# Optimization experiments

Measured on AMD Instinct MI355X. Metric: run time of the kernel, lower is better.

Reference implementation:

```python
import jax, jax.numpy as jnp
import numpy as np

N = 262144
D = 128
E = 524288
N_PHYS = 5
EPS_SL = 1e-8
EPS_LN = 1e-5


def _signed_log(x):
    return jnp.sign(x) * jnp.log(jnp.abs(x) + EPS_SL)


def setup_inputs() -> dict:
    key = jax.random.key(0)
    ks = jax.random.split(key, 12)
    h = jax.random.normal(ks[0], (N, D), dtype=jnp.float32)
    c1 = jax.random.normal(ks[1], (N,), dtype=jnp.float32)
    c2 = jax.random.normal(ks[2], (N,), dtype=jnp.float32)
    c3 = jax.random.normal(ks[3], (N,), dtype=jnp.float32)
    c4 = jax.random.normal(ks[4], (N,), dtype=jnp.float32)
    q_new = jax.random.normal(ks[5], (N,), dtype=jnp.float32)
    src = jax.random.randint(ks[6], (E,), 0, N, dtype=jnp.int64)
    dst = jax.random.randint(ks[7], (E,), 0, N, dtype=jnp.int64)
    d_in = 2 * D + N_PHYS
    W1 = jax.random.normal(ks[8], (d_in, D), dtype=jnp.float32) / np.sqrt(d_in)
    b1 = jnp.zeros((D,), dtype=jnp.float32)
    W2 = jax.random.normal(ks[9], (D, D), dtype=jnp.float32) / np.sqrt(D)
    b2 = jnp.zeros((D,), dtype=jnp.float32)
    gamma = jnp.ones((D,), dtype=jnp.float32)
    beta = jnp.zeros((D,), dtype=jnp.float32)
    return {"h": h, "c1_next_upstream": c1, "c2_prev_upstream": c2,
            "c3_self": c3, "c4_lateral": c4, "q_new": q_new,
            "src": src, "dst": dst,
            "W1": W1, "b1": b1, "W2": W2, "b2": b2,
            "gamma": gamma, "beta": beta}


def reference(h, c1_next_upstream, c2_prev_upstream, c3_self, c4_lateral,
              q_new, src, dst, W1, b1, W2, b2, gamma, beta):
    # sparse adjacency matmul: upstream_h[i] = sum_{j: j->i} h[j]
    upstream_h = jax.ops.segment_sum(h[src], dst, num_segments=h.shape[0])
    phys = jnp.stack([_signed_log(c1_next_upstream),
                      _signed_log(c2_prev_upstream),
                      _signed_log(c3_self),
                      _signed_log(c4_lateral),
                      _signed_log(q_new)], axis=-1)  # (N, 5)
    node_input = jnp.concatenate([h, upstream_h, phys], axis=-1)  # (N, 2D+5)
    hid = jax.nn.silu(node_input @ W1 + b1)
    mlp_out = hid @ W2 + b2
    z = h + mlp_out
    mean = jnp.mean(z, axis=-1, keepdims=True)
    var = jnp.var(z, axis=-1, keepdims=True)
    return (z - mean) * jax.lax.rsqrt(var + EPS_LN) * gamma + beta
```

## Files before the change

kernel.cpp:

```cpp
#include <hip/hip_runtime.h>
#include <math.h>

#define NN 262144
#define DD 128
#define EPS_SL 1e-8f
#define EPS_LN 1e-5f
#define THREADS 512
#define TILE_M 64
#define NBLOCKS 256
#define NTILES (NN / TILE_M)
#define TPB (NTILES / NBLOCKS)

typedef __attribute__((ext_vector_type(8))) short bf16x8;
typedef __attribute__((ext_vector_type(4))) float f32x4;

#define OFF_W1 0
#define OFF_W2 73728
#define OFF_X  106496
#define OFF_H  143360
#define OFF_RED 159744
#define SMEM_TOT 161792

#define WS_OFFS   0
#define WS_CURSOR 1048832
#define WS_BSUM   2097408
#define WS_ESRC   2101504
#define WS_NEEDED (2101504 + 524288 * 4)

__device__ inline unsigned short f2bf(float f) {
    union { float f; unsigned int i; } v; v.f = f;
    unsigned int r = v.i + 0x7fffu + ((v.i >> 16) & 1u);
    return (unsigned short)(r >> 16);
}
__device__ inline unsigned int pack2(float a, float b) {
    return (unsigned int)f2bf(a) | ((unsigned int)f2bf(b) << 16);
}
__device__ inline uint4 pack8(float4 a, float4 b) {
    return make_uint4(pack2(a.x, a.y), pack2(a.z, a.w),
                      pack2(b.x, b.y), pack2(b.z, b.w));
}
__device__ inline float signed_log(float x) {
    float l = __logf(fabsf(x) + EPS_SL);
    return (x > 0.f) ? l : ((x < 0.f) ? -l : 0.f);
}
__device__ inline void stx(unsigned short* sX, int kb, int row, uint4 v) {
    *(uint4*)(sX + (((kb * 64 + row) ^ (kb & 7)) * 8)) = v;
}
__device__ inline bf16x8 ldx(const unsigned short* sX, int kb, int row) {
    return *(const bf16x8*)(sX + (((kb * 64 + row) ^ (kb & 7)) * 8));
}

__global__ void hist_kernel(const int* __restrict__ dst, int* counts, int E) {
    int e = blockIdx.x * blockDim.x + threadIdx.x;
    if (e < E) atomicAdd(&counts[dst[e]], 1);
}

__global__ void scan_local(int* offs, int* bsum) {
    __shared__ int tmp[256];
    int t = threadIdx.x, i = blockIdx.x * 256 + t;
    int own = offs[i];
    tmp[t] = own;
    __syncthreads();
    for (int off = 1; off < 256; off <<= 1) {
        int v = (t >= off) ? tmp[t - off] : 0;
        __syncthreads();
        tmp[t] += v;
        __syncthreads();
    }
    offs[i] = tmp[t] - own;
    if (t == 255) bsum[blockIdx.x] = tmp[255];
}

__global__ void scan_bsum(int* bsum) {
    __shared__ int tmp[1024];
    int t = threadIdx.x;
    int own = bsum[t];
    tmp[t] = own;
    __syncthreads();
    for (int off = 1; off < 1024; off <<= 1) {
        int v = (t >= off) ? tmp[t - off] : 0;
        __syncthreads();
        tmp[t] += v;
        __syncthreads();
    }
    bsum[t] = tmp[t] - own;
}

__global__ void scan_fixup(int* offs, const int* __restrict__ bsum, int* cursor, int E) {
    int i = blockIdx.x * 256 + threadIdx.x;
    int v = offs[i] + bsum[i >> 8];
    offs[i] = v;
    cursor[i] = v;
    if (i == 0) offs[NN] = E;
}

__global__ void fill_kernel(const int* __restrict__ src, const int* __restrict__ dst,
                            int* cursor, int* esrc, int E) {
    int e = blockIdx.x * blockDim.x + threadIdx.x;
    if (e < E) {
        int p = atomicAdd(&cursor[dst[e]], 1);
        esrc[p] = src[e];
    }
}

__global__ __launch_bounds__(256) void gather_kernel(
    const float4* __restrict__ h4, const int* __restrict__ offs,
    const int* __restrict__ esrc, char* outb)
{
    int stride = gridDim.x * 256;
    for (int idx = blockIdx.x * 256 + threadIdx.x; idx < NN * 16; idx += stride) {
        int n = idx >> 4, c = idx & 15;
        int o0 = offs[n], o1 = offs[n + 1];
        float4 a = make_float4(0.f, 0.f, 0.f, 0.f);
        float4 b = make_float4(0.f, 0.f, 0.f, 0.f);
        for (int e = o0; e < o1; ++e) {
            const float4* hr = h4 + (size_t)esrc[e] * 32 + c * 2;
            float4 p0 = hr[0], p1 = hr[1];
            a.x += p0.x; a.y += p0.y; a.z += p0.z; a.w += p0.w;
            b.x += p1.x; b.y += p1.y; b.z += p1.z; b.w += p1.w;
        }
        *(uint4*)(outb + (size_t)n * 512 + c * 16) = pack8(a, b);
    }
}

__global__ void scatter_kernel(const float4* __restrict__ h4,
                               const int* __restrict__ src,
                               const int* __restrict__ dst,
                               float* up, int E) {
    int tid = blockIdx.x * blockDim.x + threadIdx.x;
    int e = tid >> 5;
    if (e >= E) return;
    int c = tid & 31;
    float4 v = h4[(size_t)src[e] * 32 + c];
    float* o = up + (size_t)dst[e] * DD + c * 4;
    atomicAdd(o + 0, v.x);
    atomicAdd(o + 1, v.y);
    atomicAdd(o + 2, v.z);
    atomicAdd(o + 3, v.w);
}

template <int GATHER>
__global__ __launch_bounds__(THREADS) void node_kernel(
    const float* __restrict__ h, const void* up,
    const float* __restrict__ c1, const float* __restrict__ c2,
    const float* __restrict__ c3, const float* __restrict__ c4,
    const float* __restrict__ qn,
    const float* __restrict__ W1, const float* __restrict__ b1,
    const float* __restrict__ W2, const float* __restrict__ b2,
    const float* __restrict__ gamma, const float* __restrict__ beta,
    float* out)
{
    extern __shared__ char smem[];
    unsigned short* sW1 = (unsigned short*)(smem + OFF_W1);
    unsigned short* sW2 = (unsigned short*)(smem + OFF_W2);
    unsigned short* sX  = (unsigned short*)(smem + OFF_X);
    unsigned short* sH  = (unsigned short*)(smem + OFF_H);
    float2* red = (float2*)(smem + OFF_RED);

    const int tid = threadIdx.x;

    for (int c = tid; c < 36 * 128; c += THREADS) {
        int kb = c >> 7, n = c & 127;
        unsigned short tmp[8] __attribute__((aligned(16)));
        #pragma unroll
        for (int j = 0; j < 8; ++j) {
            int k = kb * 8 + j;
            tmp[j] = (k < 261) ? f2bf(W1[k * DD + n]) : (unsigned short)0;
        }
        *(uint4*)(sW1 + c * 8) = *(const uint4*)tmp;
    }
    for (int c = tid; c < 16 * 128; c += THREADS) {
        int kb = c >> 7, n = c & 127;
        unsigned short tmp[8] __attribute__((aligned(16)));
        #pragma unroll
        for (int j = 0; j < 8; ++j) tmp[j] = f2bf(W2[(kb * 8 + j) * DD + n]);
        *(uint4*)(sW2 + c * 8) = *(const uint4*)tmp;
    }
    if (tid < 192) {
        int kb = 33 + (tid >> 6), row = tid & 63;
        stx(sX, kb, row, make_uint4(0u, 0u, 0u, 0u));
    }

    const int lane = tid & 63;
    const int w    = tid >> 6;
    const int wm   = w >> 2;
    const int wn   = w & 3;
    const int l15  = lane & 15;
    const int lk   = lane >> 4;
    const int col0 = wn * 32 + l15;
    const int col1 = col0 + 16;

    const float b1v[2] = {b1[col0], b1[col1]};
    const float b2v[2] = {b2[col0], b2[col1]};
    const float gv[2]  = {gamma[col0], gamma[col1]};
    const float bv[2]  = {beta[col0], beta[col1]};

    const bf16x8* W1f = (const bf16x8*)sW1;
    const bf16x8* Hf  = (const bf16x8*)sH;
    const bf16x8* W2f = (const bf16x8*)sW2;

    const int k0 = tid & 15;
    const int r0 = tid >> 4;

    float4 h0a, h0b, h1a, h1b;
    uint4  u0, u1;
    float4 v0a, v0b, v1a, v1b;
    float pc1 = 0.f, pc2 = 0.f, pc3 = 0.f, pc4 = 0.f, pc5 = 0.f;

    {
        int base = blockIdx.x * TPB * TILE_M;
        const float* hp = h + (size_t)(base + r0) * DD + k0 * 8;
        h0a = *(const float4*)hp;       h0b = *(const float4*)(hp + 4);
        h1a = *(const float4*)(hp + 32 * DD); h1b = *(const float4*)(hp + 32 * DD + 4);
        if (GATHER) {
            const char* ub = (const char*)up;
            u0 = *(const uint4*)(ub + (size_t)(base + r0) * 512 + k0 * 16);
            u1 = *(const uint4*)(ub + (size_t)(base + r0 + 32) * 512 + k0 * 16);
        } else {
            const float* uf = (const float*)up + (size_t)(base + r0) * DD + k0 * 8;
            v0a = *(const float4*)uf;       v0b = *(const float4*)(uf + 4);
            v1a = *(const float4*)(uf + 32 * DD); v1b = *(const float4*)(uf + 32 * DD + 4);
        }
        if (tid < 64) {
            int n0 = base + tid;
            pc1 = c1[n0]; pc2 = c2[n0]; pc3 = c3[n0]; pc4 = c4[n0]; pc5 = qn[n0];
        }
    }
    __syncthreads();

    for (int tt = 0; tt < TPB; ++tt) {
        const int base = (blockIdx.x * TPB + tt) * TILE_M;

        stx(sX, k0, r0,      pack8(h0a, h0b));
        stx(sX, k0, r0 + 32, pack8(h1a, h1b));
        if (GATHER) {
            stx(sX, 16 + k0, r0,      u0);
            stx(sX, 16 + k0, r0 + 32, u1);
        } else {
            stx(sX, 16 + k0, r0,      pack8(v0a, v0b));
            stx(sX, 16 + k0, r0 + 32, pack8(v1a, v1b));
        }
        if (tid < 64) {
            uint4 pv = make_uint4(pack2(signed_log(pc1), signed_log(pc2)),
                                  pack2(signed_log(pc3), signed_log(pc4)),
                                  pack2(signed_log(pc5), 0.f), 0u);
            stx(sX, 32, tid, pv);
        }

        if (tt + 1 < TPB) {
            int bn = base + TILE_M;
            const float* hp = h + (size_t)(bn + r0) * DD + k0 * 8;
            h0a = *(const float4*)hp;       h0b = *(const float4*)(hp + 4);
            h1a = *(const float4*)(hp + 32 * DD); h1b = *(const float4*)(hp + 32 * DD + 4);
            if (GATHER) {
                const char* ub = (const char*)up;
                u0 = *(const uint4*)(ub + (size_t)(bn + r0) * 512 + k0 * 16);
                u1 = *(const uint4*)(ub + (size_t)(bn + r0 + 32) * 512 + k0 * 16);
            } else {
                const float* uf = (const float*)up + (size_t)(bn + r0) * DD + k0 * 8;
                v0a = *(const float4*)uf;       v0b = *(const float4*)(uf + 4);
                v1a = *(const float4*)(uf + 32 * DD); v1b = *(const float4*)(uf + 32 * DD + 4);
            }
            if (tid < 64) {
                int n0 = bn + tid;
                pc1 = c1[n0]; pc2 = c2[n0]; pc3 = c3[n0]; pc4 = c4[n0]; pc5 = qn[n0];
            }
        }
        __syncthreads();

        f32x4 acc[2][2] = {};
        #pragma unroll
        for (int ks = 0; ks < 9; ++ks) {
            int kb = ks * 4 + lk;
            bf16x8 a0  = ldx(sX, kb, wm * 32 + l15);
            bf16x8 a1  = ldx(sX, kb, wm * 32 + 16 + l15);
            bf16x8 bb0 = W1f[kb * 128 + col0];
            bf16x8 bb1 = W1f[kb * 128 + col1];
            acc[0][0] = __builtin_amdgcn_mfma_f32_16x16x32_bf16(a0, bb0, acc[0][0], 0, 0, 0);
            acc[0][1] = __builtin_amdgcn_mfma_f32_16x16x32_bf16(a0, bb1, acc[0][1], 0, 0, 0);
            acc[1][0] = __builtin_amdgcn_mfma_f32_16x16x32_bf16(a1, bb0, acc[1][0], 0, 0, 0);
            acc[1][1] = __builtin_amdgcn_mfma_f32_16x16x32_bf16(a1, bb1, acc[1][1], 0, 0, 0);
        }
        #pragma unroll
        for (int fm = 0; fm < 2; ++fm) {
            int row = wm * 32 + fm * 16 + lk * 4;
            #pragma unroll
            for (int fn = 0; fn < 2; ++fn) {
                int col = wn * 32 + fn * 16 + l15;
                int kbh = col >> 3, ko = col & 7;
                #pragma unroll
                for (int r = 0; r < 4; ++r) {
                    float v = acc[fm][fn][r] + b1v[fn];
                    float sg = 1.f / (1.f + __expf(-v));
                    sH[(kbh * 64 + row + r) * 8 + ko] = f2bf(v * sg);
                }
            }
        }
        __syncthreads();

        f32x4 acc2[2][2] = {};
        #pragma unroll
        for (int ks = 0; ks < 4; ++ks) {
            int kb = ks * 4 + lk;
            bf16x8 a0  = Hf[kb * 64 + wm * 32 + l15];
            bf16x8 a1  = Hf[kb * 64 + wm * 32 + 16 + l15];
            bf16x8 bb0 = W2f[kb * 128 + col0];
            bf16x8 bb1 = W2f[kb * 128 + col1];
            acc2[0][0] = __builtin_amdgcn_mfma_f32_16x16x32_bf16(a0, bb0, acc2[0][0], 0, 0, 0);
            acc2[0][1] = __builtin_amdgcn_mfma_f32_16x16x32_bf16(a0, bb1, acc2[0][1], 0, 0, 0);
            acc2[1][0] = __builtin_amdgcn_mfma_f32_16x16x32_bf16(a1, bb0, acc2[1][0], 0, 0, 0);
            acc2[1][1] = __builtin_amdgcn_mfma_f32_16x16x32_bf16(a1, bb1, acc2[1][1], 0, 0, 0);
        }

        float rs1[2][4], rs2[2][4];
        #pragma unroll
        for (int fm = 0; fm < 2; ++fm) {
            #pragma unroll
            for (int r = 0; r < 4; ++r) {
                size_t rowg = (size_t)(base + wm * 32 + fm * 16 + lk * 4 + r) * DD;
                float z0 = acc2[fm][0][r] + b2v[0] + h[rowg + col0];
                float z1 = acc2[fm][1][r] + b2v[1] + h[rowg + col1];
                acc2[fm][0][r] = z0; acc2[fm][1][r] = z1;
                float s = z0 + z1, q = z0 * z0 + z1 * z1;
                #pragma unroll
                for (int off = 1; off < 16; off <<= 1) {
                    s += __shfl_xor(s, off);
                    q += __shfl_xor(q, off);
                }
                rs1[fm][r] = s; rs2[fm][r] = q;
            }
        }
        if (l15 == 0) {
            #pragma unroll
            for (int fm = 0; fm < 2; ++fm)
                #pragma unroll
                for (int r = 0; r < 4; ++r)
                    red[wn * 64 + wm * 32 + fm * 16 + lk * 4 + r] =
                        make_float2(rs1[fm][r], rs2[fm][r]);
        }
        __syncthreads();

        #pragma unroll
        for (int fm = 0; fm < 2; ++fm) {
            #pragma unroll
            for (int r = 0; r < 4; ++r) {
                int rloc = wm * 32 + fm * 16 + lk * 4 + r;
                float2 t0 = red[rloc], t1 = red[64 + rloc],
                       t2 = red[128 + rloc], t3 = red[192 + rloc];
                float S = t0.x + t1.x + t2.x + t3.x;
                float Q = t0.y + t1.y + t2.y + t3.y;
                float mean = S * (1.f / 128.f);
                float var  = Q * (1.f / 128.f) - mean * mean;
                float rstd = rsqrtf(var + EPS_LN);
                size_t rowg = (size_t)(base + rloc) * DD;
                out[rowg + col0] = (acc2[fm][0][r] - mean) * rstd * gv[0] + bv[0];
                out[rowg + col1] = (acc2[fm][1][r] - mean) * rstd * gv[1] + bv[1];
            }
        }
    }
}

extern "C" void kernel_launch(void* const* d_in, const int* in_sizes, int n_in,
                              void* d_out, int out_size, void* d_ws, size_t ws_size,
                              hipStream_t stream) {
    const float* h     = (const float*)d_in[0];
    const float* c1    = (const float*)d_in[1];
    const float* c2    = (const float*)d_in[2];
    const float* c3    = (const float*)d_in[3];
    const float* c4    = (const float*)d_in[4];
    const float* qn    = (const float*)d_in[5];
    const int*   src   = (const int*)d_in[6];
    const int*   dst   = (const int*)d_in[7];
    const float* W1    = (const float*)d_in[8];
    const float* b1    = (const float*)d_in[9];
    const float* W2    = (const float*)d_in[10];
    const float* b2    = (const float*)d_in[11];
    const float* gamma = (const float*)d_in[12];
    const float* beta  = (const float*)d_in[13];
    float* out = (float*)d_out;
    int E = in_sizes[6];

    if (ws_size >= (size_t)WS_NEEDED) {
        char* ws = (char*)d_ws;
        int* offs   = (int*)(ws + WS_OFFS);
        int* cursor = (int*)(ws + WS_CURSOR);
        int* bsum   = (int*)(ws + WS_BSUM);
        int* esrc   = (int*)(ws + WS_ESRC);

        hipMemsetAsync(offs, 0, (size_t)NN * sizeof(int), stream);
        int eb = (E + 255) / 256;
        hist_kernel<<<eb, 256, 0, stream>>>(dst, offs, E);
        scan_local<<<NN / 256, 256, 0, stream>>>(offs, bsum);
        scan_bsum<<<1, 1024, 0, stream>>>(bsum);
        scan_fixup<<<NN / 256, 256, 0, stream>>>(offs, bsum, cursor, E);
        fill_kernel<<<eb, 256, 0, stream>>>(src, dst, cursor, esrc, E);

        gather_kernel<<<2048, 256, 0, stream>>>((const float4*)h, offs, esrc, (char*)d_out);

        hipFuncSetAttribute(reinterpret_cast<const void*>(&node_kernel<1>),
                            hipFuncAttributeMaxDynamicSharedMemorySize, SMEM_TOT);
        node_kernel<1><<<NBLOCKS, THREADS, SMEM_TOT, stream>>>(
            h, d_out, c1, c2, c3, c4, qn,
            W1, b1, W2, b2, gamma, beta, out);
    } else {
        hipMemsetAsync(d_out, 0, (size_t)NN * DD * sizeof(float), stream);
        int sthreads = E * 32;
        int sblocks = (sthreads + 255) / 256;
        scatter_kernel<<<sblocks, 256, 0, stream>>>((const float4*)h, src, dst, out, E);
        hipFuncSetAttribute(reinterpret_cast<const void*>(&node_kernel<0>),
                            hipFuncAttributeMaxDynamicSharedMemorySize, SMEM_TOT);
        node_kernel<0><<<NBLOCKS, THREADS, SMEM_TOT, stream>>>(
            h, d_out, c1, c2, c3, c4, qn,
            W1, b1, W2, b2, gamma, beta, out);
    }
}
```

Measured before the change: 232.6 us.

## Fuse CSR gather into node kernel and read pre-packed weights from global

Moves the per-node neighbour gather into the node kernel, so each block first sums its 512 nodes' neighbour rows into the bf16 staging area of the output buffer and then runs the MLP on them, removing a separate kernel launch. A new prep kernel converts W1/W2 to bf16 MFMA fragments once in workspace, and the MLP reads them from global/L2 instead of each block rebuilding them in LDS. LDS use drops from about 158KB to 54KB, allowing several blocks per CU (launch bounds 4) and 512 blocks. The cost is that weight fragments are now fetched from cache on every tile, and the gather phase no longer overlaps with the matmul within a block.

Measured after the change: 363.6 us. 1.56x slower.

```diff
diff --git a/kernel.cpp b/kernel.cpp
--- a/kernel.cpp
+++ b/kernel.cpp
@@ -7,25 +7,31 @@
 #define EPS_LN 1e-5f
 #define THREADS 512
 #define TILE_M 64
-#define NBLOCKS 256
-#define NTILES (NN / TILE_M)
-#define TPB (NTILES / NBLOCKS)
+#define NBLOCKS 512
+#define TPB 8
+#define NPB (TPB * TILE_M)
 
 typedef __attribute__((ext_vector_type(8))) short bf16x8;
 typedef __attribute__((ext_vector_type(4))) float f32x4;
 
-#define OFF_W1 0
-#define OFF_W2 73728
-#define OFF_X  106496
-#define OFF_H  143360
-#define OFF_RED 159744
-#define SMEM_TOT 161792
+#define OFF_X   0
+#define OFF_H   36864
+#define OFF_RED 53248
+#define SMEM_TOT 55296
+
+#define FB_OFF_W1 0
+#define FB_OFF_W2 73728
+#define FB_OFF_X  106496
+#define FB_OFF_H  143360
+#define FB_OFF_RED 159744
+#define FB_SMEM_TOT 161792
 
 #define WS_OFFS   0
 #define WS_CURSOR 1048832
 #define WS_BSUM   2097408
 #define WS_ESRC   2101504
-#define WS_NEEDED (2101504 + 524288 * 4)
+#define WS_WFRAG  4198656
+#define WS_NEEDED (4198656 + 106496)
 
 __device__ inline unsigned short f2bf(float f) {
     union { float f; unsigned int i; } v; v.f = f;
@@ -103,24 +109,24 @@
     }
 }
 
-__global__ __launch_bounds__(256) void gather_kernel(
-    const float4* __restrict__ h4, const int* __restrict__ offs,
-    const int* __restrict__ esrc, char* outb)
-{
-    int stride = gridDim.x * 256;
-    for (int idx = blockIdx.x * 256 + threadIdx.x; idx < NN * 16; idx += stride) {
-        int n = idx >> 4, c = idx & 15;
-        int o0 = offs[n], o1 = offs[n + 1];
-        float4 a = make_float4(0.f, 0.f, 0.f, 0.f);
-        float4 b = make_float4(0.f, 0.f, 0.f, 0.f);
-        for (int e = o0; e < o1; ++e) {
-            const float4* hr = h4 + (size_t)esrc[e] * 32 + c * 2;
-            float4 p0 = hr[0], p1 = hr[1];
-            a.x += p0.x; a.y += p0.y; a.z += p0.z; a.w += p0.w;
-            b.x += p1.x; b.y += p1.y; b.z += p1.z; b.w += p1.w;
-        }
-        *(uint4*)(outb + (size_t)n * 512 + c * 16) = pack8(a, b);
-    }
+__global__ void prep_weights(const float* __restrict__ W1, const float* __restrict__ W2,
+                             uint4* wfrag) {
+    int t = blockIdx.x * blockDim.x + threadIdx.x;
+    if (t >= 52 * 128) return;
+    int kb = t >> 7, n = t & 127;
+    unsigned short tmp[8] __attribute__((aligned(16)));
+    if (kb < 36) {
+        #pragma unroll
+        for (int j = 0; j < 8; ++j) {
+            int k = kb * 8 + j;
+            tmp[j] = (k < 261) ? f2bf(W1[k * DD + n]) : (unsigned short)0;
+        }
+    } else {
+        int kb2 = kb - 36;
+        #pragma unroll
+        for (int j = 0; j < 8; ++j) tmp[j] = f2bf(W2[(kb2 * 8 + j) * DD + n]);
+    }
+    wfrag[t] = *(const uint4*)tmp;
 }
 
 __global__ void scatter_kernel(const float4* __restrict__ h4,
@@ -139,9 +145,210 @@
     atomicAdd(o + 3, v.w);
 }
 
-template <int GATHER>
-__global__ __launch_bounds__(THREADS) void node_kernel(
-    const float* __restrict__ h, const void* up,
+__global__ __launch_bounds__(THREADS, 4) void node_kernel(
+    const float* __restrict__ h,
+    const int* __restrict__ offs, const int* __restrict__ esrc,
+    const uint4* __restrict__ wfrag,
+    const float* __restrict__ c1, const float* __restrict__ c2,
+    const float* __restrict__ c3, const float* __restrict__ c4,
+    const float* __restrict__ qn,
+    const float* __restrict__ b1, const float* __restrict__ b2,
+    const float* __restrict__ gamma, const float* __restrict__ beta,
+    float* out)
+{
+    extern __shared__ char smem[];
+    unsigned short* sX = (unsigned short*)(smem + OFF_X);
+    unsigned short* sH = (unsigned short*)(smem + OFF_H);
+    float2* red = (float2*)(smem + OFF_RED);
+
+    const int tid = threadIdx.x;
+    const int nbase = blockIdx.x * NPB;
+
+    if (tid < 192) stx(sX, 33 + (tid >> 6), tid & 63, make_uint4(0u, 0u, 0u, 0u));
+
+    {
+        char* outb = (char*)out;
+        for (int it = 0; it < NPB * 16 / THREADS; ++it) {
+            int idx = it * THREADS + tid;
+            int nl = idx >> 4, c = idx & 15;
+            int n = nbase + nl;
+            int o0 = offs[n], o1 = offs[n + 1];
+            float4 a = make_float4(0.f, 0.f, 0.f, 0.f);
+            float4 b = make_float4(0.f, 0.f, 0.f, 0.f);
+            for (int e = o0; e < o1; ++e) {
+                const float4* hr = (const float4*)h + (size_t)esrc[e] * 32 + c * 2;
+                float4 p0 = hr[0], p1 = hr[1];
+                a.x += p0.x; a.y += p0.y; a.z += p0.z; a.w += p0.w;
+                b.x += p1.x; b.y += p1.y; b.z += p1.z; b.w += p1.w;
+            }
+            *(uint4*)(outb + (size_t)n * 512 + c * 16) = pack8(a, b);
+        }
+    }
+    __syncthreads();
+
+    const int lane = tid & 63;
+    const int w    = tid >> 6;
+    const int wm   = w >> 2;
+    const int wn   = w & 3;
+    const int l15  = lane & 15;
+    const int lk   = lane >> 4;
+    const int col0 = wn * 32 + l15;
+    const int col1 = col0 + 16;
+
+    const float b1v[2] = {b1[col0], b1[col1]};
+    const float b2v[2] = {b2[col0], b2[col1]};
+    const float gv[2]  = {gamma[col0], gamma[col1]};
+    const float bv[2]  = {beta[col0], beta[col1]};
+
+    const int k0 = tid & 15;
+    const int r0 = tid >> 4;
+
+    float4 h0a, h0b, h1a, h1b;
+    uint4  u0, u1;
+    float pc1 = 0.f, pc2 = 0.f, pc3 = 0.f, pc4 = 0.f, pc5 = 0.f;
+
+    {
+        int base = nbase;
+        const float* hp = h + (size_t)(base + r0) * DD + k0 * 8;
+        h0a = *(const float4*)hp;             h0b = *(const float4*)(hp + 4);
+        h1a = *(const float4*)(hp + 32 * DD); h1b = *(const float4*)(hp + 32 * DD + 4);
+        const char* ub = (const char*)out;
+        u0 = *(const uint4*)(ub + (size_t)(base + r0) * 512 + k0 * 16);
+        u1 = *(const uint4*)(ub + (size_t)(base + r0 + 32) * 512 + k0 * 16);
+        if (tid < 64) {
+            int n0 = base + tid;
+            pc1 = c1[n0]; pc2 = c2[n0]; pc3 = c3[n0]; pc4 = c4[n0]; pc5 = qn[n0];
+        }
+    }
+
+    for (int tt = 0; tt < TPB; ++tt) {
+        const int base = nbase + tt * TILE_M;
+
+        stx(sX, k0, r0,      pack8(h0a, h0b));
+        stx(sX, k0, r0 + 32, pack8(h1a, h1b));
+        stx(sX, 16 + k0, r0,      u0);
+        stx(sX, 16 + k0, r0 + 32, u1);
+        if (tid < 64) {
+            uint4 pv = make_uint4(pack2(signed_log(pc1), signed_log(pc2)),
+                                  pack2(signed_log(pc3), signed_log(pc4)),
+                                  pack2(signed_log(pc5), 0.f), 0u);
+            stx(sX, 32, tid, pv);
+        }
+
+        if (tt + 1 < TPB) {
+            int bn = base + TILE_M;
+            const float* hp = h + (size_t)(bn + r0) * DD + k0 * 8;
+            h0a = *(const float4*)hp;             h0b = *(const float4*)(hp + 4);
+            h1a = *(const float4*)(hp + 32 * DD); h1b = *(const float4*)(hp + 32 * DD + 4);
+            const char* ub = (const char*)out;
+            u0 = *(const uint4*)(ub + (size_t)(bn + r0) * 512 + k0 * 16);
+            u1 = *(const uint4*)(ub + (size_t)(bn + r0 + 32) * 512 + k0 * 16);
+            if (tid < 64) {
+                int n0 = bn + tid;
+                pc1 = c1[n0]; pc2 = c2[n0]; pc3 = c3[n0]; pc4 = c4[n0]; pc5 = qn[n0];
+            }
+        }
+        __syncthreads();
+
+        int zoff = 0;
+        asm volatile("" : "+v"(zoff));
+        const uint4* wf1 = wfrag + zoff;
+        const uint4* wf2 = wfrag + 36 * 128 + zoff;
+
+        f32x4 acc[2][2] = {};
+        #pragma unroll
+        for (int ks = 0; ks < 9; ++ks) {
+            int kb = ks * 4 + lk;
+            bf16x8 a0  = ldx(sX, kb, wm * 32 + l15);
+            bf16x8 a1  = ldx(sX, kb, wm * 32 + 16 + l15);
+            bf16x8 bb0 = *(const bf16x8*)(wf1 + kb * 128 + col0);
+            bf16x8 bb1 = *(const bf16x8*)(wf1 + kb * 128 + col1);
+            acc[0][0] = __builtin_amdgcn_mfma_f32_16x16x32_bf16(a0, bb0, acc[0][0], 0, 0, 0);
+            acc[0][1] = __builtin_amdgcn_mfma_f32_16x16x32_bf16(a0, bb1, acc[0][1], 0, 0, 0);
+            acc[1][0] = __builtin_amdgcn_mfma_f32_16x16x32_bf16(a1, bb0, acc[1][0], 0, 0, 0);
+            acc[1][1] = __builtin_amdgcn_mfma_f32_16x16x32_bf16(a1, bb1, acc[1][1], 0, 0, 0);
+        }
+        #pragma unroll
+        for (int fm = 0; fm < 2; ++fm) {
+            int row = wm * 32 + fm * 16 + lk * 4;
+            #pragma unroll
+            for (int fn = 0; fn < 2; ++fn) {
+                int col = wn * 32 + fn * 16 + l15;
+                int kbh = col >> 3, ko = col & 7;
+                #pragma unroll
+                for (int r = 0; r < 4; ++r) {
+                    float v = acc[fm][fn][r] + b1v[fn];
+                    float sg = 1.f / (1.f + __expf(-v));
+                    sH[(kbh * 64 + row + r) * 8 + ko] = f2bf(v * sg);
+                }
+            }
+        }
+        __syncthreads();
+
+        f32x4 acc2[2][2] = {};
+        #pragma unroll
+        for (int ks = 0; ks < 4; ++ks) {
+            int kb = ks * 4 + lk;
+            bf16x8 a0  = *(const bf16x8*)(sH + (kb * 64 + wm * 32 + l15) * 8);
+            bf16x8 a1  = *(const bf16x8*)(sH + (kb * 64 + wm * 32 + 16 + l15) * 8);
+            bf16x8 bb0 = *(const bf16x8*)(wf2 + kb * 128 + col0);
+            bf16x8 bb1 = *(const bf16x8*)(wf2 + kb * 128 + col1);
+            acc2[0][0] = __builtin_amdgcn_mfma_f32_16x16x32_bf16(a0, bb0, acc2[0][0], 0, 0, 0);
+            acc2[0][1] = __builtin_amdgcn_mfma_f32_16x16x32_bf16(a0, bb1, acc2[0][1], 0, 0, 0);
+            acc2[1][0] = __builtin_amdgcn_mfma_f32_16x16x32_bf16(a1, bb0, acc2[1][0], 0, 0, 0);
+            acc2[1][1] = __builtin_amdgcn_mfma_f32_16x16x32_bf16(a1, bb1, acc2[1][1], 0, 0, 0);
+        }
+
+        float rs1[2][4], rs2[2][4];
+        #pragma unroll
+        for (int fm = 0; fm < 2; ++fm) {
+            #pragma unroll
+            for (int r = 0; r < 4; ++r) {
+                size_t rowg = (size_t)(base + wm * 32 + fm * 16 + lk * 4 + r) * DD;
+                float z0 = acc2[fm][0][r] + b2v[0] + h[rowg + col0];
+                float z1 = acc2[fm][1][r] + b2v[1] + h[rowg + col1];
+                acc2[fm][0][r] = z0; acc2[fm][1][r] = z1;
+                float s = z0 + z1, q = z0 * z0 + z1 * z1;
+                #pragma unroll
+                for (int off = 1; off < 16; off <<= 1) {
+                    s += __shfl_xor(s, off);
+                    q += __shfl_xor(q, off);
+                }
+                rs1[fm][r] = s; rs2[fm][r] = q;
+            }
+        }
+        if (l15 == 0) {
+            #pragma unroll
+            for (int fm = 0; fm < 2; ++fm)
+                #pragma unroll
+                for (int r = 0; r < 4; ++r)
+                    red[wn * 64 + wm * 32 + fm * 16 + lk * 4 + r] =
+                        make_float2(rs1[fm][r], rs2[fm][r]);
+        }
+        __syncthreads();
+
+        #pragma unroll
+        for (int fm = 0; fm < 2; ++fm) {
+            #pragma unroll
+            for (int r = 0; r < 4; ++r) {
+                int rloc = wm * 32 + fm * 16 + lk * 4 + r;
+                float2 t0 = red[rloc], t1 = red[64 + rloc],
+                       t2 = red[128 + rloc], t3 = red[192 + rloc];
+                float S = t0.x + t1.x + t2.x + t3.x;
+                float Q = t0.y + t1.y + t2.y + t3.y;
+                float mean = S * (1.f / 128.f);
+                float var  = Q * (1.f / 128.f) - mean * mean;
+                float rstd = rsqrtf(var + EPS_LN);
+                size_t rowg = (size_t)(base + rloc) * DD;
+                out[rowg + col0] = (acc2[fm][0][r] - mean) * rstd * gv[0] + bv[0];
+                out[rowg + col1] = (acc2[fm][1][r] - mean) * rstd * gv[1] + bv[1];
+            }
+        }
+    }
+}
+
+__global__ __launch_bounds__(THREADS) void node_kernel_fb(
+    const float* __restrict__ h, const float* up,
     const float* __restrict__ c1, const float* __restrict__ c2,
     const float* __restrict__ c3, const float* __restrict__ c4,
     const float* __restrict__ qn,
@@ -151,11 +358,11 @@
     float* out)
 {
     extern __shared__ char smem[];
-    unsigned short* sW1 = (unsigned short*)(smem + OFF_W1);
-    unsigned short* sW2 = (unsigned short*)(smem + OFF_W2);
-    unsigned short* sX  = (unsigned short*)(smem + OFF_X);
-    unsigned short* sH  = (unsigned short*)(smem + OFF_H);
-    float2* red = (float2*)(smem + OFF_RED);
+    unsigned short* sW1 = (unsigned short*)(smem + FB_OFF_W1);
+    unsigned short* sW2 = (unsigned short*)(smem + FB_OFF_W2);
+    unsigned short* sX  = (unsigned short*)(smem + FB_OFF_X);
+    unsigned short* sH  = (unsigned short*)(smem + FB_OFF_H);
+    float2* red = (float2*)(smem + FB_OFF_RED);
 
     const int tid = threadIdx.x;
 
@@ -201,26 +408,20 @@
 
     const int k0 = tid & 15;
     const int r0 = tid >> 4;
+    const int FB_TPB = NN / TILE_M / NBLOCKS;
 
     float4 h0a, h0b, h1a, h1b;
-    uint4  u0, u1;
     float4 v0a, v0b, v1a, v1b;
     float pc1 = 0.f, pc2 = 0.f, pc3 = 0.f, pc4 = 0.f, pc5 = 0.f;
 
     {
-        int base = blockIdx.x * TPB * TILE_M;
+        int base = blockIdx.x * FB_TPB * TILE_M;
         const float* hp = h + (size_t)(base + r0) * DD + k0 * 8;
-        h0a = *(const float4*)hp;       h0b = *(const float4*)(hp + 4);
+        h0a = *(const float4*)hp;             h0b = *(const float4*)(hp + 4);
         h1a = *(const float4*)(hp + 32 * DD); h1b = *(const float4*)(hp + 32 * DD + 4);
-        if (GATHER) {
-            const char* ub = (const char*)up;
-            u0 = *(const uint4*)(ub + (size_t)(base + r0) * 512 + k0 * 16);
-            u1 = *(const uint4*)(ub + (size_t)(base + r0 + 32) * 512 + k0 * 16);
-        } else {
-            const float* uf = (const float*)up + (size_t)(base + r0) * DD + k0 * 8;
-            v0a = *(const float4*)uf;       v0b = *(const float4*)(uf + 4);
-            v1a = *(const float4*)(uf + 32 * DD); v1b = *(const float4*)(uf + 32 * DD + 4);
-        }
+        const float* uf = up + (size_t)(base + r0) * DD + k0 * 8;
+        v0a = *(const float4*)uf;             v0b = *(const float4*)(uf + 4);
+        v1a = *(const float4*)(uf + 32 * DD); v1b = *(const float4*)(uf + 32 * DD + 4);
         if (tid < 64) {
             int n0 = base + tid;
             pc1 = c1[n0]; pc2 = c2[n0]; pc3 = c3[n0]; pc4 = c4[n0]; pc5 = qn[n0];
@@ -228,39 +429,27 @@
     }
     __syncthreads();
 
-    for (int tt = 0; tt < TPB; ++tt) {
-        const int base = (blockIdx.x * TPB + tt) * TILE_M;
+    for (int tt = 0; tt < FB_TPB; ++tt) {
+        const int base = (blockIdx.x * FB_TPB + tt) * TILE_M;
 
         stx(sX, k0, r0,      pack8(h0a, h0b));
         stx(sX, k0, r0 + 32, pack8(h1a, h1b));
-        if (GATHER) {
-            stx(sX, 16 + k0, r0,      u0);
-            stx(sX, 16 + k0, r0 + 32, u1);
-        } else {
-            stx(sX, 16 + k0, r0,      pack8(v0a, v0b));
-            stx(sX, 16 + k0, r0 + 32, pack8(v1a, v1b));
-        }
+        stx(sX, 16 + k0, r0,      pack8(v0a, v0b));
+        stx(sX, 16 + k0, r0 + 32, pack8(v1a, v1b));
         if (tid < 64) {
             uint4 pv = make_uint4(pack2(signed_log(pc1), signed_log(pc2)),
                                   pack2(signed_log(pc3), signed_log(pc4)),
                                   pack2(signed_log(pc5), 0.f), 0u);
             stx(sX, 32, tid, pv);
         }
-
-        if (tt + 1 < TPB) {
+        if (tt + 1 < FB_TPB) {
             int bn = base + TILE_M;
             const float* hp = h + (size_t)(bn + r0) * DD + k0 * 8;
-            h0a = *(const float4*)hp;       h0b = *(const float4*)(hp + 4);
+            h0a = *(const float4*)hp;             h0b = *(const float4*)(hp + 4);
             h1a = *(const float4*)(hp + 32 * DD); h1b = *(const float4*)(hp + 32 * DD + 4);
-            if (GATHER) {
-                const char* ub = (const char*)up;
-                u0 = *(const uint4*)(ub + (size_t)(bn + r0) * 512 + k0 * 16);
-                u1 = *(const uint4*)(ub + (size_t)(bn + r0 + 32) * 512 + k0 * 16);
-            } else {
-                const float* uf = (const float*)up + (size_t)(bn + r0) * DD + k0 * 8;
-                v0a = *(const float4*)uf;       v0b = *(const float4*)(uf + 4);
-                v1a = *(const float4*)(uf + 32 * DD); v1b = *(const float4*)(uf + 32 * DD + 4);
-            }
+            const float* uf = up + (size_t)(bn + r0) * DD + k0 * 8;
+            v0a = *(const float4*)uf;             v0b = *(const float4*)(uf + 4);
+            v1a = *(const float4*)(uf + 32 * DD); v1b = *(const float4*)(uf + 32 * DD + 4);
             if (tid < 64) {
                 int n0 = bn + tid;
                 pc1 = c1[n0]; pc2 = c2[n0]; pc3 = c3[n0]; pc4 = c4[n0]; pc5 = qn[n0];
@@ -386,6 +575,7 @@
         int* cursor = (int*)(ws + WS_CURSOR);
         int* bsum   = (int*)(ws + WS_BSUM);
         int* esrc   = (int*)(ws + WS_ESRC);
+        uint4* wfrag = (uint4*)(ws + WS_WFRAG);
 
         hipMemsetAsync(offs, 0, (size_t)NN * sizeof(int), stream);
         int eb = (E + 255) / 256;
@@ -394,23 +584,20 @@
         scan_bsum<<<1, 1024, 0, stream>>>(bsum);
         scan_fixup<<<NN / 256, 256, 0, stream>>>(offs, bsum, cursor, E);
         fill_kernel<<<eb, 256, 0, stream>>>(src, dst, cursor, esrc, E);
-
-        gather_kernel<<<2048, 256, 0, stream>>>((const float4*)h, offs, esrc, (char*)d_out);
-
-        hipFuncSetAttribute(reinterpret_cast<const void*>(&node_kernel<1>),
-                            hipFuncAttributeMaxDynamicSharedMemorySize, SMEM_TOT);
-        node_kernel<1><<<NBLOCKS, THREADS, SMEM_TOT, stream>>>(
-            h, d_out, c1, c2, c3, c4, qn,
-            W1, b1, W2, b2, gamma, beta, out);
+        prep_weights<<<26, 256, 0, stream>>>(W1, W2, wfrag);
+
+        node_kernel<<<NBLOCKS, THREADS, SMEM_TOT, stream>>>(
+            h, offs, esrc, wfrag, c1, c2, c3, c4, qn,
+            b1, b2, gamma, beta, out);
     } else {
         hipMemsetAsync(d_out, 0, (size_t)NN * DD * sizeof(float), stream);
         int sthreads = E * 32;
         int sblocks = (sthreads + 255) / 256;
         scatter_kernel<<<sblocks, 256, 0, stream>>>((const float4*)h, src, dst, out, E);
-        hipFuncSetAttribute(reinterpret_cast<const void*>(&node_kernel<0>),
-                            hipFuncAttributeMaxDynamicSharedMemorySize, SMEM_TOT);
-        node_kernel<0><<<NBLOCKS, THREADS, SMEM_TOT, stream>>>(
-            h, d_out, c1, c2, c3, c4, qn,
+        hipFuncSetAttribute(reinterpret_cast<const void*>(&node_kernel_fb),
+                            hipFuncAttributeMaxDynamicSharedMemorySize, FB_SMEM_TOT);
+        node_kernel_fb<<<NBLOCKS, THREADS, FB_SMEM_TOT, stream>>>(
+            h, out, c1, c2, c3, c4, qn,
             W1, b1, W2, b2, gamma, beta, out);
     }
 }
```

## Double node kernel threads to 1024 with one 16-row MFMA strip per wave

Applied to the files above, without the earlier changes.

Raises the node kernel block size from 512 to 1024 threads so each of the 16 waves handles a 16-row by 32-column fragment instead of 32 rows. Each thread now loads one row-chunk of h and upstream rather than two. The work per wave is halved to expose more parallelism and latency hiding within the block. In exchange there is less B-operand reuse per wave, the W1/W2 fragments are re-read from LDS by more waves, and there are more waves per barrier. Two further edits are not about speed: the workspace size check now derives from E, and launch bounds gain a minimum-blocks hint.

Result: slower. 241.9 us (+4.0%).

```diff
diff --git a/kernel.cpp b/kernel.cpp
--- a/kernel.cpp
+++ b/kernel.cpp
@@ -5,7 +5,7 @@
 #define DD 128
 #define EPS_SL 1e-8f
 #define EPS_LN 1e-5f
-#define THREADS 512
+#define THREADS 1024
 #define TILE_M 64
 #define NBLOCKS 256
 #define NTILES (NN / TILE_M)
@@ -25,7 +25,6 @@
 #define WS_CURSOR 1048832
 #define WS_BSUM   2097408
 #define WS_ESRC   2101504
-#define WS_NEEDED (2101504 + 524288 * 4)
 
 __device__ inline unsigned short f2bf(float f) {
     union { float f; unsigned int i; } v; v.f = f;
@@ -140,7 +139,7 @@
 }
 
 template <int GATHER>
-__global__ __launch_bounds__(THREADS) void node_kernel(
+__global__ __launch_bounds__(THREADS, 4) void node_kernel(
     const float* __restrict__ h, const void* up,
     const float* __restrict__ c1, const float* __restrict__ c2,
     const float* __restrict__ c3, const float* __restrict__ c4,
@@ -202,24 +201,21 @@
     const int k0 = tid & 15;
     const int r0 = tid >> 4;
 
-    float4 h0a, h0b, h1a, h1b;
-    uint4  u0, u1;
-    float4 v0a, v0b, v1a, v1b;
+    float4 h0a, h0b;
+    uint4  u0;
+    float4 v0a, v0b;
     float pc1 = 0.f, pc2 = 0.f, pc3 = 0.f, pc4 = 0.f, pc5 = 0.f;
 
     {
         int base = blockIdx.x * TPB * TILE_M;
         const float* hp = h + (size_t)(base + r0) * DD + k0 * 8;
-        h0a = *(const float4*)hp;       h0b = *(const float4*)(hp + 4);
-        h1a = *(const float4*)(hp + 32 * DD); h1b = *(const float4*)(hp + 32 * DD + 4);
+        h0a = *(const float4*)hp; h0b = *(const float4*)(hp + 4);
         if (GATHER) {
             const char* ub = (const char*)up;
             u0 = *(const uint4*)(ub + (size_t)(base + r0) * 512 + k0 * 16);
-            u1 = *(const uint4*)(ub + (size_t)(base + r0 + 32) * 512 + k0 * 16);
         } else {
             const float* uf = (const float*)up + (size_t)(base + r0) * DD + k0 * 8;
-            v0a = *(const float4*)uf;       v0b = *(const float4*)(uf + 4);
-            v1a = *(const float4*)(uf + 32 * DD); v1b = *(const float4*)(uf + 32 * DD + 4);
+            v0a = *(const float4*)uf; v0b = *(const float4*)(uf + 4);
         }
         if (tid < 64) {
             int n0 = base + tid;
@@ -231,15 +227,9 @@
     for (int tt = 0; tt < TPB; ++tt) {
         const int base = (blockIdx.x * TPB + tt) * TILE_M;
 
-        stx(sX, k0, r0,      pack8(h0a, h0b));
-        stx(sX, k0, r0 + 32, pack8(h1a, h1b));
-        if (GATHER) {
-            stx(sX, 16 + k0, r0,      u0);
-            stx(sX, 16 + k0, r0 + 32, u1);
-        } else {
-            stx(sX, 16 + k0, r0,      pack8(v0a, v0b));
-            stx(sX, 16 + k0, r0 + 32, pack8(v1a, v1b));
-        }
+        stx(sX, k0, r0, pack8(h0a, h0b));
+        if (GATHER) stx(sX, 16 + k0, r0, u0);
+        else        stx(sX, 16 + k0, r0, pack8(v0a, v0b));
         if (tid < 64) {
             uint4 pv = make_uint4(pack2(signed_log(pc1), signed_log(pc2)),
                                   pack2(signed_log(pc3), signed_log(pc4)),
@@ -250,16 +240,13 @@
         if (tt + 1 < TPB) {
             int bn = base + TILE_M;
             const float* hp = h + (size_t)(bn + r0) * DD + k0 * 8;
-            h0a = *(const float4*)hp;       h0b = *(const float4*)(hp + 4);
-            h1a = *(const float4*)(hp + 32 * DD); h1b = *(const float4*)(hp + 32 * DD + 4);
+            h0a = *(const float4*)hp; h0b = *(const float4*)(hp + 4);
             if (GATHER) {
                 const char* ub = (const char*)up;
                 u0 = *(const uint4*)(ub + (size_t)(bn + r0) * 512 + k0 * 16);
-                u1 = *(const uint4*)(ub + (size_t)(bn + r0 + 32) * 512 + k0 * 16);
             } else {
                 const float* uf = (const float*)up + (size_t)(bn + r0) * DD + k0 * 8;
-                v0a = *(const float4*)uf;       v0b = *(const float4*)(uf + 4);
-                v1a = *(const float4*)(uf + 32 * DD); v1b = *(const float4*)(uf + 32 * DD + 4);
+                v0a = *(const float4*)uf; v0b = *(const float4*)(uf + 4);
             }
             if (tid < 64) {
                 int n0 = bn + tid;
@@ -268,29 +255,25 @@
         }
         __syncthreads();
 
-        f32x4 acc[2][2] = {};
+        f32x4 acc[2] = {};
         #pragma unroll
         for (int ks = 0; ks < 9; ++ks) {
             int kb = ks * 4 + lk;
-            bf16x8 a0  = ldx(sX, kb, wm * 32 + l15);
-            bf16x8 a1  = ldx(sX, kb, wm * 32 + 16 + l15);
+            bf16x8 a   = ldx(sX, kb, wm * 16 + l15);
             bf16x8 bb0 = W1f[kb * 128 + col0];
             bf16x8 bb1 = W1f[kb * 128 + col1];
-            acc[0][0] = __builtin_amdgcn_mfma_f32_16x16x32_bf16(a0, bb0, acc[0][0], 0, 0, 0);
-            acc[0][1] = __builtin_amdgcn_mfma_f32_16x16x32_bf16(a0, bb1, acc[0][1], 0, 0, 0);
-            acc[1][0] = __builtin_amdgcn_mfma_f32_16x16x32_bf16(a1, bb0, acc[1][0], 0, 0, 0);
-            acc[1][1] = __builtin_amdgcn_mfma_f32_16x16x32_bf16(a1, bb1, acc[1][1], 0, 0, 0);
-        }
-        #pragma unroll
-        for (int fm = 0; fm < 2; ++fm) {
-            int row = wm * 32 + fm * 16 + lk * 4;
+            acc[0] = __builtin_amdgcn_mfma_f32_16x16x32_bf16(a, bb0, acc[0], 0, 0, 0);
+            acc[1] = __builtin_amdgcn_mfma_f32_16x16x32_bf16(a, bb1, acc[1], 0, 0, 0);
+        }
+        {
+            int row = wm * 16 + lk * 4;
             #pragma unroll
             for (int fn = 0; fn < 2; ++fn) {
                 int col = wn * 32 + fn * 16 + l15;
                 int kbh = col >> 3, ko = col & 7;
                 #pragma unroll
                 for (int r = 0; r < 4; ++r) {
-                    float v = acc[fm][fn][r] + b1v[fn];
+                    float v = acc[fn][r] + b1v[fn];
                     float sg = 1.f / (1.f + __expf(-v));
                     sH[(kbh * 64 + row + r) * 8 + ko] = f2bf(v * sg);
                 }
@@ -298,64 +281,52 @@
         }
         __syncthreads();
 
-        f32x4 acc2[2][2] = {};
+        f32x4 acc2[2] = {};
         #pragma unroll
         for (int ks = 0; ks < 4; ++ks) {
             int kb = ks * 4 + lk;
-            bf16x8 a0  = Hf[kb * 64 + wm * 32 + l15];
-            bf16x8 a1  = Hf[kb * 64 + wm * 32 + 16 + l15];
+            bf16x8 a   = Hf[kb * 64 + wm * 16 + l15];
             bf16x8 bb0 = W2f[kb * 128 + col0];
             bf16x8 bb1 = W2f[kb * 128 + col1];
-            acc2[0][0] = __builtin_amdgcn_mfma_f32_16x16x32_bf16(a0, bb0, acc2[0][0], 0, 0, 0);
-            acc2[0][1] = __builtin_amdgcn_mfma_f32_16x16x32_bf16(a0, bb1, acc2[0][1], 0, 0, 0);
-            acc2[1][0] = __builtin_amdgcn_mfma_f32_16x16x32_bf16(a1, bb0, acc2[1][0], 0, 0, 0);
-            acc2[1][1] = __builtin_amdgcn_mfma_f32_16x16x32_bf16(a1, bb1, acc2[1][1], 0, 0, 0);
-        }
-
-        float rs1[2][4], rs2[2][4];
-        #pragma unroll
-        for (int fm = 0; fm < 2; ++fm) {
+            acc2[0] = __builtin_amdgcn_mfma_f32_16x16x32_bf16(a, bb0, acc2[0], 0, 0, 0);
+            acc2[1] = __builtin_amdgcn_mfma_f32_16x16x32_bf16(a, bb1, acc2[1], 0, 0, 0);
+        }
+
+        float rs1[4], rs2[4];
+        #pragma unroll
+        for (int r = 0; r < 4; ++r) {
+            size_t rowg = (size_t)(base + wm * 16 + lk * 4 + r) * DD;
+            float z0 = acc2[0][r] + b2v[0] + h[rowg + col0];
+            float z1 = acc2[1][r] + b2v[1] + h[rowg + col1];
+            acc2[0][r] = z0; acc2[1][r] = z1;
+            float s = z0 + z1, q = z0 * z0 + z1 * z1;
             #pragma unroll
-            for (int r = 0; r < 4; ++r) {
-                size_t rowg = (size_t)(base + wm * 32 + fm * 16 + lk * 4 + r) * DD;
-                float z0 = acc2[fm][0][r] + b2v[0] + h[rowg + col0];
-                float z1 = acc2[fm][1][r] + b2v[1] + h[rowg + col1];
-                acc2[fm][0][r] = z0; acc2[fm][1][r] = z1;
-                float s = z0 + z1, q = z0 * z0 + z1 * z1;
-                #pragma unroll
-                for (int off = 1; off < 16; off <<= 1) {
-                    s += __shfl_xor(s, off);
-                    q += __shfl_xor(q, off);
-                }
-                rs1[fm][r] = s; rs2[fm][r] = q;
+            for (int off = 1; off < 16; off <<= 1) {
+                s += __shfl_xor(s, off);
+                q += __shfl_xor(q, off);
             }
+            rs1[r] = s; rs2[r] = q;
         }
         if (l15 == 0) {
             #pragma unroll
-            for (int fm = 0; fm < 2; ++fm)
-                #pragma unroll
-                for (int r = 0; r < 4; ++r)
-                    red[wn * 64 + wm * 32 + fm * 16 + lk * 4 + r] =
-                        make_float2(rs1[fm][r], rs2[fm][r]);
-        }
-        __syncthreads();
-
-        #pragma unroll
-        for (int fm = 0; fm < 2; ++fm) {
-            #pragma unroll
-            for (int r = 0; r < 4; ++r) {
-                int rloc = wm * 32 + fm * 16 + lk * 4 + r;
-                float2 t0 = red[rloc], t1 = red[64 + rloc],
-                       t2 = red[128 + rloc], t3 = red[192 + rloc];
-                float S = t0.x + t1.x + t2.x + t3.x;
-                float Q = t0.y + t1.y + t2.y + t3.y;
-                float mean = S * (1.f / 128.f);
-                float var  = Q * (1.f / 128.f) - mean * mean;
-                float rstd = rsqrtf(var + EPS_LN);
-                size_t rowg = (size_t)(base + rloc) * DD;
-                out[rowg + col0] = (acc2[fm][0][r] - mean) * rstd * gv[0] + bv[0];
-                out[rowg + col1] = (acc2[fm][1][r] - mean) * rstd * gv[1] + bv[1];
-            }
+            for (int r = 0; r < 4; ++r)
+                red[wn * 64 + wm * 16 + lk * 4 + r] = make_float2(rs1[r], rs2[r]);
+        }
+        __syncthreads();
+
+        #pragma unroll
+        for (int r = 0; r < 4; ++r) {
+            int rloc = wm * 16 + lk * 4 + r;
+            float2 t0 = red[rloc], t1 = red[64 + rloc],
+                   t2 = red[128 + rloc], t3 = red[192 + rloc];
+            float S = t0.x + t1.x + t2.x + t3.x;
+            float Q = t0.y + t1.y + t2.y + t3.y;
+            float mean = S * (1.f / 128.f);
+            float var  = Q * (1.f / 128.f) - mean * mean;
+            float rstd = rsqrtf(var + EPS_LN);
+            size_t rowg = (size_t)(base + rloc) * DD;
+            out[rowg + col0] = (acc2[0][r] - mean) * rstd * gv[0] + bv[0];
+            out[rowg + col1] = (acc2[1][r] - mean) * rstd * gv[1] + bv[1];
         }
     }
 }
@@ -379,8 +350,9 @@
     const float* beta  = (const float*)d_in[13];
     float* out = (float*)d_out;
     int E = in_sizes[6];
-
-    if (ws_size >= (size_t)WS_NEEDED) {
+    size_t ws_needed = (size_t)WS_ESRC + (size_t)E * 4;
+
+    if (ws_size >= ws_needed) {
         char* ws = (char*)d_ws;
         int* offs   = (int*)(ws + WS_OFFS);
         int* cursor = (int*)(ws + WS_CURSOR);
```

## Pack bf16 h alongside gathered sums; read residual from shared memory

Applied to the files above, without the earlier changes.

The gather kernel now also writes a bf16 copy of each node's own h row into the second half of its 512-byte output slot, which previously went unused. The node kernel then loads both halves from that staging buffer instead of reading fp32 h twice (once for the MLP input, once for the residual). The residual is now read back from the bf16 tile in shared memory. This cuts global reads in the node kernel at the cost of extra h reads and writes in the gather pass, and the residual loses precision by using bf16 instead of fp32 h.

Result: slower. 261.4 us (+12.4%).

```diff
diff --git a/kernel.cpp b/kernel.cpp
--- a/kernel.cpp
+++ b/kernel.cpp
@@ -25,13 +25,15 @@
 #define WS_CURSOR 1048832
 #define WS_BSUM   2097408
 #define WS_ESRC   2101504
-#define WS_NEEDED (2101504 + 524288 * 4)
 
 __device__ inline unsigned short f2bf(float f) {
     union { float f; unsigned int i; } v; v.f = f;
     unsigned int r = v.i + 0x7fffu + ((v.i >> 16) & 1u);
     return (unsigned short)(r >> 16);
 }
+__device__ inline float bf2f(unsigned short u) {
+    union { float f; unsigned int i; } v; v.i = ((unsigned int)u) << 16; return v.f;
+}
 __device__ inline unsigned int pack2(float a, float b) {
     return (unsigned int)f2bf(a) | ((unsigned int)f2bf(b) << 16);
 }
@@ -48,6 +50,9 @@
 }
 __device__ inline bf16x8 ldx(const unsigned short* sX, int kb, int row) {
     return *(const bf16x8*)(sX + (((kb * 64 + row) ^ (kb & 7)) * 8));
+}
+__device__ inline float ldx_elem(const unsigned short* sX, int kb, int row, int e) {
+    return bf2f(sX[(((kb * 64 + row) ^ (kb & 7)) * 8) + e]);
 }
 
 __global__ void hist_kernel(const int* __restrict__ dst, int* counts, int E) {
@@ -119,7 +124,11 @@
             a.x += p0.x; a.y += p0.y; a.z += p0.z; a.w += p0.w;
             b.x += p1.x; b.y += p1.y; b.z += p1.z; b.w += p1.w;
         }
-        *(uint4*)(outb + (size_t)n * 512 + c * 16) = pack8(a, b);
+        const float4* hn = h4 + (size_t)n * 32 + c * 2;
+        float4 q0 = hn[0], q1 = hn[1];
+        char* slot = outb + (size_t)n * 512;
+        *(uint4*)(slot + c * 16)       = pack8(a, b);
+        *(uint4*)(slot + 256 + c * 16) = pack8(q0, q1);
     }
 }
 
@@ -202,23 +211,25 @@
     const int k0 = tid & 15;
     const int r0 = tid >> 4;
 
+    uint4 hu0, hu1, uu0, uu1;
     float4 h0a, h0b, h1a, h1b;
-    uint4  u0, u1;
     float4 v0a, v0b, v1a, v1b;
     float pc1 = 0.f, pc2 = 0.f, pc3 = 0.f, pc4 = 0.f, pc5 = 0.f;
 
     {
         int base = blockIdx.x * TPB * TILE_M;
-        const float* hp = h + (size_t)(base + r0) * DD + k0 * 8;
-        h0a = *(const float4*)hp;       h0b = *(const float4*)(hp + 4);
-        h1a = *(const float4*)(hp + 32 * DD); h1b = *(const float4*)(hp + 32 * DD + 4);
         if (GATHER) {
             const char* ub = (const char*)up;
-            u0 = *(const uint4*)(ub + (size_t)(base + r0) * 512 + k0 * 16);
-            u1 = *(const uint4*)(ub + (size_t)(base + r0 + 32) * 512 + k0 * 16);
+            const char* s0 = ub + (size_t)(base + r0) * 512 + k0 * 16;
+            const char* s1 = ub + (size_t)(base + r0 + 32) * 512 + k0 * 16;
+            uu0 = *(const uint4*)s0;  hu0 = *(const uint4*)(s0 + 256);
+            uu1 = *(const uint4*)s1;  hu1 = *(const uint4*)(s1 + 256);
         } else {
+            const float* hp = h + (size_t)(base + r0) * DD + k0 * 8;
+            h0a = *(const float4*)hp;             h0b = *(const float4*)(hp + 4);
+            h1a = *(const float4*)(hp + 32 * DD); h1b = *(const float4*)(hp + 32 * DD + 4);
             const float* uf = (const float*)up + (size_t)(base + r0) * DD + k0 * 8;
-            v0a = *(const float4*)uf;       v0b = *(const float4*)(uf + 4);
+            v0a = *(const float4*)uf;             v0b = *(const float4*)(uf + 4);
             v1a = *(const float4*)(uf + 32 * DD); v1b = *(const float4*)(uf + 32 * DD + 4);
         }
         if (tid < 64) {
@@ -231,12 +242,14 @@
     for (int tt = 0; tt < TPB; ++tt) {
         const int base = (blockIdx.x * TPB + tt) * TILE_M;
 
-        stx(sX, k0, r0,      pack8(h0a, h0b));
-        stx(sX, k0, r0 + 32, pack8(h1a, h1b));
         if (GATHER) {
-            stx(sX, 16 + k0, r0,      u0);
-            stx(sX, 16 + k0, r0 + 32, u1);
+            stx(sX, k0, r0,           hu0);
+            stx(sX, k0, r0 + 32,      hu1);
+            stx(sX, 16 + k0, r0,      uu0);
+            stx(sX, 16 + k0, r0 + 32, uu1);
         } else {
+            stx(sX, k0, r0,           pack8(h0a, h0b));
+            stx(sX, k0, r0 + 32,      pack8(h1a, h1b));
             stx(sX, 16 + k0, r0,      pack8(v0a, v0b));
             stx(sX, 16 + k0, r0 + 32, pack8(v1a, v1b));
         }
@@ -249,16 +262,18 @@
 
         if (tt + 1 < TPB) {
             int bn = base + TILE_M;
-            const float* hp = h + (size_t)(bn + r0) * DD + k0 * 8;
-            h0a = *(const float4*)hp;       h0b = *(const float4*)(hp + 4);
-            h1a = *(const float4*)(hp + 32 * DD); h1b = *(const float4*)(hp + 32 * DD + 4);
             if (GATHER) {
                 const char* ub = (const char*)up;
-                u0 = *(const uint4*)(ub + (size_t)(bn + r0) * 512 + k0 * 16);
-                u1 = *(const uint4*)(ub + (size_t)(bn + r0 + 32) * 512 + k0 * 16);
+                const char* s0 = ub + (size_t)(bn + r0) * 512 + k0 * 16;
+                const char* s1 = ub + (size_t)(bn + r0 + 32) * 512 + k0 * 16;
+                uu0 = *(const uint4*)s0;  hu0 = *(const uint4*)(s0 + 256);
+                uu1 = *(const uint4*)s1;  hu1 = *(const uint4*)(s1 + 256);
             } else {
+                const float* hp = h + (size_t)(bn + r0) * DD + k0 * 8;
+                h0a = *(const float4*)hp;             h0b = *(const float4*)(hp + 4);
+                h1a = *(const float4*)(hp + 32 * DD); h1b = *(const float4*)(hp + 32 * DD + 4);
                 const float* uf = (const float*)up + (size_t)(bn + r0) * DD + k0 * 8;
-                v0a = *(const float4*)uf;       v0b = *(const float4*)(uf + 4);
+                v0a = *(const float4*)uf;             v0b = *(const float4*)(uf + 4);
                 v1a = *(const float4*)(uf + 32 * DD); v1b = *(const float4*)(uf + 32 * DD + 4);
             }
             if (tid < 64) {
@@ -312,14 +327,25 @@
             acc2[1][1] = __builtin_amdgcn_mfma_f32_16x16x32_bf16(a1, bb1, acc2[1][1], 0, 0, 0);
         }
 
+        const int kbc0 = col0 >> 3, ec0 = col0 & 7;
+        const int kbc1 = col1 >> 3, ec1 = col1 & 7;
         float rs1[2][4], rs2[2][4];
         #pragma unroll
         for (int fm = 0; fm < 2; ++fm) {
             #pragma unroll
             for (int r = 0; r < 4; ++r) {
-                size_t rowg = (size_t)(base + wm * 32 + fm * 16 + lk * 4 + r) * DD;
-                float z0 = acc2[fm][0][r] + b2v[0] + h[rowg + col0];
-                float z1 = acc2[fm][1][r] + b2v[1] + h[rowg + col1];
+                int rloc = wm * 32 + fm * 16 + lk * 4 + r;
+                float hres0, hres1;
+                if (GATHER) {
+                    hres0 = ldx_elem(sX, kbc0, rloc, ec0);
+                    hres1 = ldx_elem(sX, kbc1, rloc, ec1);
+                } else {
+                    size_t rowg = (size_t)(base + rloc) * DD;
+                    hres0 = h[rowg + col0];
+                    hres1 = h[rowg + col1];
+                }
+                float z0 = acc2[fm][0][r] + b2v[0] + hres0;
+                float z1 = acc2[fm][1][r] + b2v[1] + hres1;
                 acc2[fm][0][r] = z0; acc2[fm][1][r] = z1;
                 float s = z0 + z1, q = z0 * z0 + z1 * z1;
                 #pragma unroll
@@ -379,8 +405,9 @@
     const float* beta  = (const float*)d_in[13];
     float* out = (float*)d_out;
     int E = in_sizes[6];
-
-    if (ws_size >= (size_t)WS_NEEDED) {
+    size_t ws_needed = (size_t)WS_ESRC + (size_t)E * 4;
+
+    if (ws_size >= ws_needed) {
         char* ws = (char*)d_ws;
         int* offs   = (int*)(ws + WS_OFFS);
         int* cursor = (int*)(ws + WS_CURSOR);
```
